# Performance work log

Measured on AMD Instinct MI355X. Metric: run time of the kernel, lower is better.

The kernel has to match this reference:

```python
import jax, jax.numpy as jnp
import numpy as np

B, H, IN, OUT = 64, 512, 256, 256


def setup_inputs() -> dict:
    key = jax.random.key(0)
    ks = jax.random.split(key, 12)
    inputs = jax.random.normal(ks[0], (B, IN), dtype=jnp.float32)
    prev = jax.random.normal(ks[1], (B, H), dtype=jnp.float32)
    hebb = jax.random.uniform(ks[2], (B, H, H), dtype=jnp.float32) * 0.1
    # learned parameters (mirror torch init scales)
    w = 0.01 * jax.random.uniform(ks[3], (H, H), dtype=jnp.float32)
    alpha = 0.01 * jax.random.uniform(ks[4], (H, H), dtype=jnp.float32)
    eta = jnp.full((1,), 0.01, dtype=jnp.float32)
    Wi = jax.random.normal(ks[5], (H, IN), dtype=jnp.float32) / np.sqrt(IN)
    bi = jnp.zeros((H,), dtype=jnp.float32)
    Wo = jax.random.normal(ks[6], (OUT, H), dtype=jnp.float32) / np.sqrt(H)
    bo = jnp.zeros((OUT,), dtype=jnp.float32)
    Wv = jax.random.normal(ks[7], (1, H), dtype=jnp.float32) / np.sqrt(H)
    bv = jnp.zeros((1,), dtype=jnp.float32)
    return {"inputs": inputs, "prev": prev, "hebb": hebb, "w": w, "alpha": alpha,
            "eta": eta, "Wi": Wi, "bi": bi, "Wo": Wo, "bo": bo, "Wv": Wv, "bv": bv}


def reference(inputs, prev, hebb, w, alpha, eta, Wi, bi, Wo, bo, Wv, bv):
    # input projection: fc_i2h(inputs) -> [B, H]
    pre = inputs @ Wi.T + bi
    # per-batch plastic weight matvec: (w + alpha*hebb) @ prev  -> [B, H]
    rec = jnp.einsum('bij,bj->bi', w[None, :, :] + alpha[None, :, :] * hebb, prev)
    hidden = jnp.tanh(pre + rec)                      # [B, H]
    a_out = hidden @ Wo.T + bo                        # [B, OUT]
    v_out = hidden @ Wv.T + bv                        # [B, 1]
    # Hebbian outer-product trace update with clamp
    delta = hidden[:, :, None] * prev[:, None, :]     # [B, H, H]
    hebb_new = jnp.clip(hebb + eta[0] * delta, -1.0, 1.0)
    return (a_out, v_out, hidden, hebb_new)
```

## Files before the change

### kernel.cpp

```cpp
#include <hip/hip_runtime.h>
#include <math.h>

#define BB 64
#define HH 512
#define IN_DIM 256
#define OUT_DIM 256

typedef float f4 __attribute__((ext_vector_type(4)));

__device__ __forceinline__ float fast_tanh(float x) {
    const float ax = fabsf(x);
    const float e  = __expf(2.f * ax);
    const float t  = 1.f - 2.f / (e + 1.f);
    return copysignf(t, x);
}

__device__ __forceinline__ f4 clamp1(f4 v) {
    return __builtin_elementwise_min(__builtin_elementwise_max(v, (f4)(-1.f)), (f4)(1.f));
}

__global__ __launch_bounds__(256, 4) void fused_row_kernel(
    const float* __restrict__ inputs, const float* __restrict__ prev,
    const float* __restrict__ hebb,   const float* __restrict__ w,
    const float* __restrict__ alpha,  const float* __restrict__ eta,
    const float* __restrict__ Wi,     const float* __restrict__ bi,
    float* __restrict__ hidden, float* __restrict__ hebb_new)
{
    const int wid4 = (blockIdx.x * 256 + threadIdx.x) >> 6;
    const int lane = threadIdx.x & 63;
    const int b  = wid4 & (BB - 1);
    const int i0 = (wid4 >> 6) * 4;

    const int j0 = lane * 4;
    const int j1 = j0 + 256;

    const float* prow = prev + (size_t)b * HH;
    const f4 p0 = *(const f4*)(prow + j0);
    const f4 p1 = *(const f4*)(prow + j1);
    const f4 xv = *(const f4*)(inputs + (size_t)b * IN_DIM + j0);

    const size_t rbase = ((size_t)b * HH + i0) * HH;

    f4 h0[4], h1[4];
    #pragma unroll
    for (int r = 0; r < 4; ++r) {
        h0[r] = *(const f4*)(hebb + rbase + (size_t)r * HH + j0);
        h1[r] = *(const f4*)(hebb + rbase + (size_t)r * HH + j1);
    }

    float acc[4];
    #pragma unroll
    for (int r = 0; r < 4; ++r) {
        const size_t wo = (size_t)(i0 + r) * HH;
        const f4 w0 = *(const f4*)(w + wo + j0);
        const f4 w1 = *(const f4*)(w + wo + j1);
        const f4 a0 = *(const f4*)(alpha + wo + j0);
        const f4 a1 = *(const f4*)(alpha + wo + j1);
        f4 v = (w0 + a0 * h0[r]) * p0 + (w1 + a1 * h1[r]) * p1;
        const f4 wi = *(const f4*)(Wi + (size_t)(i0 + r) * IN_DIM + j0);
        v += wi * xv;
        acc[r] = v.x + v.y + v.z + v.w;
    }

    #pragma unroll
    for (int d = 32; d > 0; d >>= 1) {
        acc[0] += __shfl_xor(acc[0], d, 64);
        acc[1] += __shfl_xor(acc[1], d, 64);
        acc[2] += __shfl_xor(acc[2], d, 64);
        acc[3] += __shfl_xor(acc[3], d, 64);
    }

    const float et = eta[0];
    const float hv0 = fast_tanh(acc[0] + bi[i0]);
    const float hv1 = fast_tanh(acc[1] + bi[i0 + 1]);
    const float hv2 = fast_tanh(acc[2] + bi[i0 + 2]);
    const float hv3 = fast_tanh(acc[3] + bi[i0 + 3]);

    if (lane == 0) {
        f4 hvv; hvv.x = hv0; hvv.y = hv1; hvv.z = hv2; hvv.w = hv3;
        *(f4*)(hidden + (size_t)b * HH + i0) = hvv;
    }

    const float e0 = et * hv0, e1 = et * hv1, e2 = et * hv2, e3 = et * hv3;

    *(f4*)(hebb_new + rbase + 0 * HH + j0) = clamp1(h0[0] + e0 * p0);
    *(f4*)(hebb_new + rbase + 0 * HH + j1) = clamp1(h1[0] + e0 * p1);
    *(f4*)(hebb_new + rbase + 1 * HH + j0) = clamp1(h0[1] + e1 * p0);
    *(f4*)(hebb_new + rbase + 1 * HH + j1) = clamp1(h1[1] + e1 * p1);
    *(f4*)(hebb_new + rbase + 2 * HH + j0) = clamp1(h0[2] + e2 * p0);
    *(f4*)(hebb_new + rbase + 2 * HH + j1) = clamp1(h1[2] + e2 * p1);
    *(f4*)(hebb_new + rbase + 3 * HH + j0) = clamp1(h0[3] + e3 * p0);
    *(f4*)(hebb_new + rbase + 3 * HH + j1) = clamp1(h1[3] + e3 * p1);
}

__global__ __launch_bounds__(256) void out_proj_kernel(
    const float* __restrict__ hidden, const float* __restrict__ Wo,
    const float* __restrict__ bo,     const float* __restrict__ Wv,
    const float* __restrict__ bv,
    float* __restrict__ a_out, float* __restrict__ v_out)
{
    const int wid  = (blockIdx.x * 256 + threadIdx.x) >> 6;
    const int lane = threadIdx.x & 63;
    const int b = wid / 257;
    const int o = wid - b * 257;

    const int j0 = lane * 4;
    const int j1 = j0 + 256;

    const float* hrow = hidden + (size_t)b * HH;
    const f4 h0 = *(const f4*)(hrow + j0);
    const f4 h1 = *(const f4*)(hrow + j1);

    const float* wrow = (o < OUT_DIM) ? (Wo + (size_t)o * HH) : Wv;
    const f4 w0 = *(const f4*)(wrow + j0);
    const f4 w1 = *(const f4*)(wrow + j1);

    const f4 pv = h0 * w0 + h1 * w1;
    float acc = pv.x + pv.y + pv.z + pv.w;

    #pragma unroll
    for (int d = 32; d > 0; d >>= 1) acc += __shfl_xor(acc, d, 64);

    if (lane == 0) {
        if (o < OUT_DIM) a_out[(size_t)b * OUT_DIM + o] = acc + bo[o];
        else             v_out[b] = acc + bv[0];
    }
}

extern "C" void kernel_launch(void* const* d_in, const int* in_sizes, int n_in,
                              void* d_out, int out_size, void* d_ws, size_t ws_size,
                              hipStream_t stream) {
    const float* inputs = (const float*)d_in[0];
    const float* prev   = (const float*)d_in[1];
    const float* hebb   = (const float*)d_in[2];
    const float* w      = (const float*)d_in[3];
    const float* alpha  = (const float*)d_in[4];
    const float* eta    = (const float*)d_in[5];
    const float* Wi     = (const float*)d_in[6];
    const float* bi     = (const float*)d_in[7];
    const float* Wo     = (const float*)d_in[8];
    const float* bo     = (const float*)d_in[9];
    const float* Wv     = (const float*)d_in[10];
    const float* bv     = (const float*)d_in[11];

    float* out      = (float*)d_out;
    float* a_out    = out;
    float* v_out    = a_out + BB * OUT_DIM;
    float* hidden   = v_out + BB;
    float* hebb_new = hidden + BB * HH;

    fused_row_kernel<<<dim3(HH / 4 * BB / 4), dim3(256), 0, stream>>>(
        inputs, prev, hebb, w, alpha, eta, Wi, bi, hidden, hebb_new);

    out_proj_kernel<<<dim3((BB * 257 + 3) / 4), dim3(256), 0, stream>>>(
        hidden, Wo, bo, Wv, bv, a_out, v_out);
}
```

Before: 32.57 us.

## Merge row and output-projection kernels into one cooperative kernel with grid sync

Replaces the two back-to-back launches with a single persistent cooperative kernel. Waves grid-stride over the Hebbian row work, then a grid-wide barrier is taken before they grid-stride over the output projection. The aim is to remove the second launch and the gap between kernels. In exchange it adds an occupancy query on every call, the cost of the grid barrier, and fewer resident waves per batch row. If the cooperative launch fails, it falls back to the old two-kernel path.

```diff
diff --git a/kernel.cpp b/kernel.cpp
--- a/kernel.cpp
+++ b/kernel.cpp
@@ -1,10 +1,13 @@
 #include <hip/hip_runtime.h>
+#include <hip/hip_cooperative_groups.h>
 #include <math.h>
 
 #define BB 64
 #define HH 512
 #define IN_DIM 256
 #define OUT_DIM 256
+
+namespace cg = cooperative_groups;
 
 typedef float f4 __attribute__((ext_vector_type(4)));
 
@@ -17,6 +20,114 @@
 
 __device__ __forceinline__ f4 clamp1(f4 v) {
     return __builtin_elementwise_min(__builtin_elementwise_max(v, (f4)(-1.f)), (f4)(1.f));
+}
+
+__global__ __launch_bounds__(256, 4) void fused_all_kernel(
+    const float* __restrict__ inputs, const float* __restrict__ prev,
+    const float* __restrict__ hebb,   const float* __restrict__ w,
+    const float* __restrict__ alpha,  const float* __restrict__ eta,
+    const float* __restrict__ Wi,     const float* __restrict__ bi,
+    const float* __restrict__ Wo,     const float* __restrict__ bo,
+    const float* __restrict__ Wv,     const float* __restrict__ bv,
+    float* __restrict__ a_out, float* __restrict__ v_out,
+    float* __restrict__ hidden, float* __restrict__ hebb_new)
+{
+    const int wgl    = (blockIdx.x * 256 + threadIdx.x) >> 6;
+    const int nwaves = (gridDim.x * 256) >> 6;
+    const int lane   = threadIdx.x & 63;
+    const int j0 = lane * 4;
+    const int j1 = j0 + 256;
+
+    {
+        const int b = wgl & (BB - 1);
+        const float* prow = prev + (size_t)b * HH;
+        const f4 p0 = *(const f4*)(prow + j0);
+        const f4 p1 = *(const f4*)(prow + j1);
+        const f4 xv = *(const f4*)(inputs + (size_t)b * IN_DIM + j0);
+        const float et = eta[0];
+
+        #pragma unroll 1
+        for (int wid4 = wgl; wid4 < BB * HH / 4; wid4 += nwaves) {
+            const int i0 = (wid4 >> 6) * 4;
+            const size_t rbase = ((size_t)b * HH + i0) * HH;
+
+            f4 h0[4], h1[4];
+            #pragma unroll
+            for (int r = 0; r < 4; ++r) {
+                h0[r] = *(const f4*)(hebb + rbase + (size_t)r * HH + j0);
+                h1[r] = *(const f4*)(hebb + rbase + (size_t)r * HH + j1);
+            }
+
+            float acc[4];
+            #pragma unroll
+            for (int r = 0; r < 4; ++r) {
+                const size_t wo = (size_t)(i0 + r) * HH;
+                const f4 w0 = *(const f4*)(w + wo + j0);
+                const f4 w1 = *(const f4*)(w + wo + j1);
+                const f4 a0 = *(const f4*)(alpha + wo + j0);
+                const f4 a1 = *(const f4*)(alpha + wo + j1);
+                f4 v = (w0 + a0 * h0[r]) * p0 + (w1 + a1 * h1[r]) * p1;
+                const f4 wi = *(const f4*)(Wi + (size_t)(i0 + r) * IN_DIM + j0);
+                v += wi * xv;
+                acc[r] = v.x + v.y + v.z + v.w;
+            }
+
+            #pragma unroll
+            for (int d = 32; d > 0; d >>= 1) {
+                acc[0] += __shfl_xor(acc[0], d, 64);
+                acc[1] += __shfl_xor(acc[1], d, 64);
+                acc[2] += __shfl_xor(acc[2], d, 64);
+                acc[3] += __shfl_xor(acc[3], d, 64);
+            }
+
+            const float hv0 = fast_tanh(acc[0] + bi[i0]);
+            const float hv1 = fast_tanh(acc[1] + bi[i0 + 1]);
+            const float hv2 = fast_tanh(acc[2] + bi[i0 + 2]);
+            const float hv3 = fast_tanh(acc[3] + bi[i0 + 3]);
+
+            if (lane == 0) {
+                f4 hvv; hvv.x = hv0; hvv.y = hv1; hvv.z = hv2; hvv.w = hv3;
+                *(f4*)(hidden + (size_t)b * HH + i0) = hvv;
+            }
+
+            const float e0 = et * hv0, e1 = et * hv1, e2 = et * hv2, e3 = et * hv3;
+            *(f4*)(hebb_new + rbase + 0 * HH + j0) = clamp1(h0[0] + e0 * p0);
+            *(f4*)(hebb_new + rbase + 0 * HH + j1) = clamp1(h1[0] + e0 * p1);
+            *(f4*)(hebb_new + rbase + 1 * HH + j0) = clamp1(h0[1] + e1 * p0);
+            *(f4*)(hebb_new + rbase + 1 * HH + j1) = clamp1(h1[1] + e1 * p1);
+            *(f4*)(hebb_new + rbase + 2 * HH + j0) = clamp1(h0[2] + e2 * p0);
+            *(f4*)(hebb_new + rbase + 2 * HH + j1) = clamp1(h1[2] + e2 * p1);
+            *(f4*)(hebb_new + rbase + 3 * HH + j0) = clamp1(h0[3] + e3 * p0);
+            *(f4*)(hebb_new + rbase + 3 * HH + j1) = clamp1(h1[3] + e3 * p1);
+        }
+    }
+
+    cg::this_grid().sync();
+
+    #pragma unroll 1
+    for (int oid = wgl; oid < BB * 257; oid += nwaves) {
+        const int b = oid / 257;
+        const int o = oid - b * 257;
+
+        const float* hrow = hidden + (size_t)b * HH;
+        const f4 h0 = *(const f4*)(hrow + j0);
+        const f4 h1 = *(const f4*)(hrow + j1);
+
+        const float* wrow = (o < OUT_DIM) ? (Wo + (size_t)o * HH) : Wv;
+        const f4 w0 = *(const f4*)(wrow + j0);
+        const f4 w1 = *(const f4*)(wrow + j1);
+
+        const f4 pv = h0 * w0 + h1 * w1;
+        float acc = pv.x + pv.y + pv.z + pv.w;
+
+        #pragma unroll
+        for (int d = 32; d > 0; d >>= 1) acc += __shfl_xor(acc, d, 64);
+
+        if (lane == 0) {
+            if (o < OUT_DIM) a_out[(size_t)b * OUT_DIM + o] = acc + bo[o];
+            else             v_out[b] = acc + bv[0];
+        }
+    }
 }
 
 __global__ __launch_bounds__(256, 4) void fused_row_kernel(
@@ -82,7 +193,6 @@
     }
 
     const float e0 = et * hv0, e1 = et * hv1, e2 = et * hv2, e3 = et * hv3;
-
     *(f4*)(hebb_new + rbase + 0 * HH + j0) = clamp1(h0[0] + e0 * p0);
     *(f4*)(hebb_new + rbase + 0 * HH + j1) = clamp1(h1[0] + e0 * p1);
     *(f4*)(hebb_new + rbase + 1 * HH + j0) = clamp1(h0[1] + e1 * p0);
@@ -149,9 +259,29 @@
     float* hidden   = v_out + BB;
     float* hebb_new = hidden + BB * HH;
 
-    fused_row_kernel<<<dim3(HH / 4 * BB / 4), dim3(256), 0, stream>>>(
-        inputs, prev, hebb, w, alpha, eta, Wi, bi, hidden, hebb_new);
-
-    out_proj_kernel<<<dim3((BB * 257 + 3) / 4), dim3(256), 0, stream>>>(
-        hidden, Wo, bo, Wv, bv, a_out, v_out);
-}
+    int max_blocks_per_cu = 0;
+    hipError_t qerr = hipOccupancyMaxActiveBlocksPerMultiprocessor(
+        &max_blocks_per_cu, (const void*)fused_all_kernel, 256, 0);
+    int grid = 1024;
+    if (qerr == hipSuccess && max_blocks_per_cu > 0) {
+        int cap = max_blocks_per_cu * 256;
+        if (cap < grid) grid = cap;
+    }
+    grid = (grid / 16) * 16;
+    if (grid < 16) grid = 16;
+
+    void* args[] = { (void*)&inputs, (void*)&prev, (void*)&hebb, (void*)&w,
+                     (void*)&alpha, (void*)&eta, (void*)&Wi, (void*)&bi,
+                     (void*)&Wo, (void*)&bo, (void*)&Wv, (void*)&bv,
+                     (void*)&a_out, (void*)&v_out, (void*)&hidden, (void*)&hebb_new };
+
+    hipError_t err = hipLaunchCooperativeKernel(
+        (const void*)fused_all_kernel, dim3(grid), dim3(256), args, 0, stream);
+
+    if (err != hipSuccess) {
+        fused_row_kernel<<<dim3(HH / 4 * BB / 4), dim3(256), 0, stream>>>(
+            inputs, prev, hebb, w, alpha, eta, Wi, bi, hidden, hebb_new);
+        out_proj_kernel<<<dim3((BB * 257 + 3) / 4), dim3(256), 0, stream>>>(
+            hidden, Wo, bo, Wv, bv, a_out, v_out);
+    }
+}
```

Result: slower. 107.4 us (+229.7%).
